# Kernel tuning notes

Measured on AMD Instinct MI355X. Metric: run time of the kernel, lower is better.

## Reference

```python
import jax, jax.numpy as jnp
import numpy as np

B, JX, JQ, D = 16, 4096, 512, 256
VERY_NEG = -1e30


def setup_inputs() -> dict:
    key = jax.random.key(0)
    ks = jax.random.split(key, 8)
    c = jax.random.normal(ks[0], (B, JX, D), dtype=jnp.float32)
    q = jax.random.normal(ks[1], (B, JQ, D), dtype=jnp.float32)
    # glorot-ish scaled weights for [4d, d] projections
    s = 1.0 / np.sqrt(4 * D)
    Wr = jax.random.normal(ks[2], (4 * D, D), dtype=jnp.float32) * s
    Wg = jax.random.normal(ks[3], (4 * D, D), dtype=jnp.float32) * s
    Br = jnp.zeros((D,), dtype=jnp.float32)
    Bg = jnp.zeros((D,), dtype=jnp.float32)
    # padding masks from random valid lengths (realistic ragged batch)
    c_len = jax.random.randint(ks[4], (B,), JX // 2, JX + 1)
    q_len = jax.random.randint(ks[5], (B,), JQ // 2, JQ + 1)
    c_mask = jnp.arange(JX)[None, :] < c_len[:, None]
    q_mask = jnp.arange(JQ)[None, :] < q_len[:, None]
    return {"c": c, "q": q, "Wr": Wr, "Br": Br, "Wg": Wg, "Bg": Bg,
            "c_mask": c_mask, "q_mask": q_mask}


def reference(c, q, Wr, Br, Wg, Bg, c_mask, q_mask):
    # logits[b,x,j] = <c[b,x], q[b,j]>
    logits = jnp.einsum('bxd,bjd->bxj', c, q)
    # exp_mask: add VERY_NEG where (c_mask & q_mask) is False
    cq_mask = c_mask[:, :, None] & q_mask[:, None, :]  # [B,JX,JQ]
    logits = logits + (1.0 - cq_mask.astype(logits.dtype)) * VERY_NEG
    a = jax.nn.softmax(logits, axis=-1)                # [B,JX,JQ]
    q_a = jnp.einsum('bxj,bjd->bxd', a, q)             # [B,JX,D]
    # semantic fusion unit
    cc = jnp.concatenate([c, q_a, c * q_a, c - q_a], axis=-1)  # [B,JX,4D]
    r_ = jnp.tanh(cc @ Wr + Br)
    g = jax.nn.sigmoid(cc @ Wg + Bg)
    return g * r_ + (1.0 - g) * c
```

## Files before the change

kernel.cpp:

```cpp
#include <hip/hip_runtime.h>
#include <hip/hip_bf16.h>
#include <stdint.h>

#define NB 16
#define JXX 4096
#define JQQ 512
#define DDD 256
#define LOG2E 1.44269504f

typedef __attribute__((ext_vector_type(8))) _Float16 f16x8;
typedef __attribute__((ext_vector_type(4))) _Float16 f16x4;
typedef __attribute__((ext_vector_type(4))) float f32x4;

__device__ __forceinline__ uint16_t f2h(float f) {
    union { _Float16 h; uint16_t s; } u; u.h = (_Float16)f; return u.s;
}
__device__ __forceinline__ float h2f(uint16_t s) {
    union { _Float16 h; uint16_t s; } u; u.s = s; return (float)u.h;
}

__device__ __forceinline__ void gload_lds16(const void* g, void* l) {
    __builtin_amdgcn_global_load_lds(
        (const __attribute__((address_space(1))) void*)g,
        (__attribute__((address_space(3))) void*)l, 16, 0, 0);
}

#define VMW(N) asm volatile("s_waitcnt vmcnt(" #N ")" ::: "memory")

__global__ void k_prep(const void* cmask, const void* qmask,
                       const float* __restrict__ qg,
                       const float* __restrict__ Wr, const float* __restrict__ Wg,
                       uint8_t* cm8, uint8_t* qm8,
                       uint16_t* __restrict__ qS, uint16_t* __restrict__ qTS,
                       uint16_t* __restrict__ WP3) {
    __shared__ __align__(16) char smem[16896];
    const int blk = blockIdx.x;
    const int t = threadIdx.x;

    if (blk < 256) {
        int i = blk * 256 + t;
        uint32_t w0c = *(const uint32_t*)cmask;
        uint32_t w0q = *(const uint32_t*)qmask;
        int mc = (w0c == 1u) ? 1 : (w0c == 0x3f800000u ? 2 : 0);
        int mq = (w0q == 1u) ? 1 : (w0q == 0x3f800000u ? 2 : 0);
        if (i < NB * JXX) {
            uint8_t v;
            if (mc == 1)      v = ((const int*)cmask)[i] != 0;
            else if (mc == 2) v = ((const float*)cmask)[i] != 0.0f;
            else              v = ((const uint8_t*)cmask)[i] != 0;
            cm8[i] = v;
        }
        if (i < NB * JQQ) {
            uint8_t v;
            if (mq == 1)      v = ((const int*)qmask)[i] != 0;
            else if (mq == 2) v = ((const float*)qmask)[i] != 0.0f;
            else              v = ((const uint8_t*)qmask)[i] != 0;
            qm8[i] = v;
        }
    } else if (blk < 768) {
        float (*tile)[65] = (float (*)[65])smem;
        const int idx = blk - 256;
        const int b = idx >> 5, jb = idx & 7, db = (idx & 31) >> 3;
        const int j0 = jb * 64, d0 = db * 64;
        #pragma unroll
        for (int i = 0; i < 16; i++) {
            int e = t + 256 * i;
            int r = e >> 6, c = e & 63;
            tile[r][c] = qg[((long)b * JQQ + j0 + r) * DDD + d0 + c];
        }
        __syncthreads();
        #pragma unroll
        for (int i = 0; i < 2; i++) {
            int e = t + 256 * i;
            int r = e >> 3, c8 = e & 7;
            f16x8 v;
            #pragma unroll
            for (int k = 0; k < 8; k++) v[k] = (_Float16)tile[r][c8 * 8 + k];
            int jt = (j0 >> 5) + (r >> 5);
            int row = r & 31;
            int d8 = (d0 >> 3) + c8;
            int byt = ((row * 512 + d8 * 16) ^ ((row & 7) << 4));
            *(f16x8*)(qS + ((long)(b * 16 + jt)) * 8192 + (byt >> 1)) = v;
        }
        #pragma unroll
        for (int i = 0; i < 2; i++) {
            int e = t + 256 * i;
            int dd = e >> 3, j8 = e & 7;
            f16x8 v;
            #pragma unroll
            for (int k = 0; k < 8; k++) v[k] = (_Float16)tile[j8 * 8 + k][dd];
            int jt = (j0 >> 5) + (j8 >> 2);
            int d = d0 + dd;
            int byt = ((d * 64 + (j8 & 3) * 16) ^ (((d >> 1) & 3) << 4));
            *(f16x8*)(qTS + ((long)(b * 16 + jt)) * 8192 + (byt >> 1)) = v;
        }
    } else {
        _Float16* tile = (_Float16*)smem;
        const int idx = blk - 768;
        const int ktl = idx & 7, rem = idx >> 3;
        const int comp = rem % 3, rg = rem / 3;
        const float* W = rg ? Wg : Wr;
        const int base0 = (comp == 0 ? 0 : comp == 1 ? 256 : 512) + ktl * 32;
        #pragma unroll
        for (int i = 0; i < 32; i++) {
            int e = t + 256 * i;
            int r = e >> 8, ccol = e & 255;
            float v = W[(long)(base0 + r) * 256 + ccol];
            if (comp == 0)      v += W[(long)(768 + ktl * 32 + r) * 256 + ccol];
            else if (comp == 1) v -= W[(long)(768 + ktl * 32 + r) * 256 + ccol];
            tile[r * 264 + ccol] = (_Float16)v;
        }
        __syncthreads();
        const int step = ktl * 3 + comp;
        #pragma unroll
        for (int ss = 0; ss < 4; ss++) {
            int slot = ss * 256 + t;
            int ntg = slot >> 6, lane = slot & 63;
            int gg = lane >> 4, l = lane & 15;
            f16x8 v;
            #pragma unroll
            for (int i = 0; i < 8; i++) v[i] = tile[(gg * 8 + i) * 264 + ntg * 16 + l];
            int hh = ntg >> 3, ntl = ntg & 7;
            long off = (long)step * 16384 + hh * 8192 + rg * 4096 + ntl * 512 + lane * 8;
            *(f16x8*)(WP3 + off) = v;
        }
    }
}

__global__ __launch_bounds__(256, 2) void k_attn(
    const float* __restrict__ cg,
    const uint16_t* __restrict__ qS,
    const uint16_t* __restrict__ qTS,
    const uint8_t* __restrict__ cm8,
    const uint8_t* __restrict__ qm8,
    uint16_t* __restrict__ qa16,
    uint16_t* __restrict__ c16)
{
    __shared__ __align__(16) uint16_t qbuf[2][8192];
    __shared__ __align__(16) uint16_t qTbuf[2][8192];
    __shared__ __align__(16) uint16_t P_lds[4 * 32 * 40];
    __shared__ __align__(16) uint32_t qm_lds[128];

    const int b = blockIdx.y;
    const int t = threadIdx.x;
    const int wave = t >> 6;
    const int lane = t & 63;
    const int l15 = lane & 15;
    const int g = lane >> 4;
    const int xw = blockIdx.x * 128 + wave * 32;

    if (t < 128) {
        uint32_t m = ((const uint32_t*)(qm8 + (long)b * JQQ))[t];
        qm_lds[t] = m;
    }

    f16x8 cfrag[2][8];
    bool cvalid[2];
    float m_run[2], s_run[2];
    #pragma unroll
    for (int xs = 0; xs < 2; xs++) {
        const long rowg = (long)b * JXX + xw + xs * 16 + l15;
        const float* crow = cg + rowg * DDD;
        uint16_t* c16row = c16 + rowg * DDD;
        #pragma unroll
        for (int kb = 0; kb < 8; kb++) {
            float4 v0 = *(const float4*)(crow + kb * 32 + g * 8);
            float4 v1 = *(const float4*)(crow + kb * 32 + g * 8 + 4);
            f16x8 f;
            f[0] = (_Float16)v0.x; f[1] = (_Float16)v0.y; f[2] = (_Float16)v0.z; f[3] = (_Float16)v0.w;
            f[4] = (_Float16)v1.x; f[5] = (_Float16)v1.y; f[6] = (_Float16)v1.z; f[7] = (_Float16)v1.w;
            cfrag[xs][kb] = f;
            *(f16x8*)(c16row + kb * 32 + g * 8) = f;
        }
        cvalid[xs] = cm8[rowg] != 0;
        m_run[xs] = cvalid[xs] ? -1e30f : 0.0f;
        s_run[xs] = 0.0f;
    }
    const f32x4 fzero = {0.f, 0.f, 0.f, 0.f};
    f32x4 qa[16][2];
    #pragma unroll
    for (int i = 0; i < 16; i++) { qa[i][0] = fzero; qa[i][1] = fzero; }

    const uint16_t* qSb  = qS  + (long)(b * 16) * 8192;
    const uint16_t* qTSb = qTS + (long)(b * 16) * 8192;

    const int kbit = (l15 >> 2) & 1;
    const int qbase = l15 * 256 + (((g * 16) ^ ((l15 & 3) << 4)) >> 1);
    const int qTbase = l15 * 32 + ((g ^ ((l15 >> 1) & 3)) * 8);

    #define STAGE_ATTN(bsel, tile)                                              \
        {                                                                       \
            const uint16_t* s1 = qSb + (long)(tile) * 8192;                     \
            const uint16_t* s2 = qTSb + (long)(tile) * 8192;                    \
            _Pragma("unroll")                                                   \
            for (int i = 0; i < 4; i++)                                         \
                gload_lds16(s1 + i * 2048 + t * 8,                              \
                            &qbuf[bsel][i * 2048 + wave * 512]);                \
            _Pragma("unroll")                                                   \
            for (int i = 0; i < 4; i++)                                         \
                gload_lds16(s2 + i * 2048 + t * 8,                              \
                            &qTbuf[bsel][i * 2048 + wave * 512]);               \
        }

    STAGE_ATTN(0, 0);
    asm volatile("s_waitcnt lgkmcnt(0)" ::: "memory");
    __builtin_amdgcn_s_barrier();

    int cur = 0;
    for (int jt = 0; jt < 16; jt++) {
        if (jt < 15) {
            STAGE_ATTN(cur ^ 1, jt + 1);
            VMW(8);
        } else {
            VMW(0);
        }
        __builtin_amdgcn_s_barrier();
        __builtin_amdgcn_sched_barrier(0);

        const uint16_t* qb_l  = &qbuf[cur][0];
        const uint16_t* qTb_l = &qTbuf[cur][0];

        uint32_t qmw[2];
        qmw[0] = qm_lds[jt * 8 + g];
        qmw[1] = qm_lds[jt * 8 + 4 + g];

        f32x4 acc[2][2];
        acc[0][0] = fzero; acc[0][1] = fzero; acc[1][0] = fzero; acc[1][1] = fzero;
        __builtin_amdgcn_s_setprio(1);
        #pragma unroll
        for (int js = 0; js < 2; js++) {
            #pragma unroll
            for (int kb = 0; kb < 8; kb++) {
                f16x8 qf = *(const f16x8*)(qb_l + js * 4096 + qbase + ((kb ^ kbit) << 5));
                acc[js][0] = __builtin_amdgcn_mfma_f32_16x16x32_f16(qf, cfrag[0][kb], acc[js][0], 0, 0, 0);
                acc[js][1] = __builtin_amdgcn_mfma_f32_16x16x32_f16(qf, cfrag[1][kb], acc[js][1], 0, 0, 0);
            }
        }
        __builtin_amdgcn_s_setprio(0);

        f16x4 pv[2][2];
        float fsc[2];
        #pragma unroll
        for (int xs = 0; xs < 2; xs++) {
            float lmax = -1e30f;
            #pragma unroll
            for (int js = 0; js < 2; js++) {
                #pragma unroll
                for (int r = 0; r < 4; r++) {
                    bool qv = (qmw[js] >> (8 * r)) & 0xffu;
                    lmax = fmaxf(lmax, qv ? acc[js][xs][r] : -1e30f);
                }
            }
            lmax = fmaxf(lmax, __shfl_xor(lmax, 16));
            lmax = fmaxf(lmax, __shfl_xor(lmax, 32));
            float m_new = cvalid[xs] ? ((lmax > m_run[xs] + 8.0f) ? lmax : m_run[xs]) : 0.0f;
            fsc[xs] = exp2f((m_run[xs] - m_new) * LOG2E);
            float psum = 0.0f;
            #pragma unroll
            for (int js = 0; js < 2; js++) {
                #pragma unroll
                for (int r = 0; r < 4; r++) {
                    bool qv = (qmw[js] >> (8 * r)) & 0xffu;
                    float p = qv ? exp2f((acc[js][xs][r] - m_new) * LOG2E) : 0.0f;
                    if (!cvalid[xs]) p = 1.0f;
                    psum += p;
                    pv[xs][js][r] = (_Float16)p;
                }
            }
            s_run[xs] = s_run[xs] * fsc[xs] + psum;
            m_run[xs] = m_new;
        }
        if (!__all(fsc[0] == 1.0f && fsc[1] == 1.0f)) {
            #pragma unroll
            for (int dt = 0; dt < 16; dt++) {
                #pragma unroll
                for (int xs = 0; xs < 2; xs++) {
                    qa[dt][xs][0] *= fsc[xs]; qa[dt][xs][1] *= fsc[xs];
                    qa[dt][xs][2] *= fsc[xs]; qa[dt][xs][3] *= fsc[xs];
                }
            }
        }

        uint16_t* Pw0 = P_lds + wave * 1280;
        #pragma unroll
        for (int xs = 0; xs < 2; xs++) {
            *(f16x4*)(Pw0 + (xs * 16 + l15) * 40 + g * 4) = pv[xs][0];
            *(f16x4*)(Pw0 + (xs * 16 + l15) * 40 + 16 + g * 4) = pv[xs][1];
        }
        f16x8 pa[2];
        pa[0] = *(const f16x8*)(Pw0 + l15 * 40 + g * 8);
        pa[1] = *(const f16x8*)(Pw0 + (16 + l15) * 40 + g * 8);

        __builtin_amdgcn_s_setprio(1);
        #pragma unroll
        for (int dt = 0; dt < 16; dt++) {
            f16x8 bq = *(const f16x8*)(qTb_l + qTbase + dt * 512);
            qa[dt][0] = __builtin_amdgcn_mfma_f32_16x16x32_f16(bq, pa[0], qa[dt][0], 0, 0, 0);
            qa[dt][1] = __builtin_amdgcn_mfma_f32_16x16x32_f16(bq, pa[1], qa[dt][1], 0, 0, 0);
        }
        __builtin_amdgcn_s_setprio(0);

        __builtin_amdgcn_sched_barrier(0);
        __builtin_amdgcn_s_barrier();
        cur ^= 1;
    }
    #undef STAGE_ATTN

    #pragma unroll
    for (int xs = 0; xs < 2; xs++) {
        float s_tot = s_run[xs] + __shfl_xor(s_run[xs], 16);
        s_tot = s_tot + __shfl_xor(s_tot, 32);
        float inv = 1.0f / s_tot;
        uint16_t* outp = qa16 + ((long)b * JXX + xw + xs * 16 + l15) * DDD;
        #pragma unroll
        for (int dt = 0; dt < 16; dt++) {
            f16x4 v;
            v[0] = (_Float16)(qa[dt][xs][0] * inv);
            v[1] = (_Float16)(qa[dt][xs][1] * inv);
            v[2] = (_Float16)(qa[dt][xs][2] * inv);
            v[3] = (_Float16)(qa[dt][xs][3] * inv);
            *(f16x4*)(outp + dt * 16 + g * 4) = v;
        }
    }
}

__global__ __launch_bounds__(256, 2) void k_sfu(
    const uint16_t* __restrict__ c16g,
    const uint16_t* __restrict__ qa16,
    const uint16_t* __restrict__ WP3,
    const float* __restrict__ Brb,
    const float* __restrict__ Bgb,
    float* __restrict__ outg)
{
    __shared__ __align__(16) uint16_t ab_lds[2][4096];
    __shared__ __align__(16) uint16_t wbuf[2][16384];

    const int t = threadIdx.x;
    const int wave = t >> 6, lane = t & 63;
    const int l15 = lane & 15, g = lane >> 4;
    const long m0 = (long)blockIdx.x * 64;

    const f32x4 fzero = {0.f, 0.f, 0.f, 0.f};
    f32x4 accR[4][4], accG[4][4];
    #pragma unroll
    for (int a = 0; a < 4; a++)
        #pragma unroll
        for (int bq = 0; bq < 4; bq++) { accR[a][bq] = fzero; accG[a][bq] = fzero; }

    const int wrd = (wave >> 1) * 8192 + (wave & 1) * 2048 + lane * 8;

    #define STAGE_CQA(dt_)                                                        \
        { _Pragma("unroll")                                                       \
          for (int j = 0; j < 2; j++) {                                           \
              int pp = j * 256 + t;                                               \
              int row = pp >> 3, pc = pp & 7;                                     \
              long src = (m0 + row) * 256 + (dt_) * 64 + ((pc ^ (row & 7)) << 3); \
              int dst = (j * 256 + wave * 64) * 8;                                \
              gload_lds16(c16g + src, &ab_lds[0][dst]);                           \
              gload_lds16(qa16 + src, &ab_lds[1][dst]);                           \
          } }

    #define STAGE_W(s_)                                                           \
        { _Pragma("unroll")                                                       \
          for (int i = 0; i < 8; i++)                                             \
              gload_lds16(WP3 + (long)(s_) * 16384 + i * 2048 + t * 8,            \
                          &wbuf[(s_) & 1][i * 2048 + wave * 512]); }

    STAGE_CQA(0);
    STAGE_W(0);
    VMW(0);
    __builtin_amdgcn_s_barrier();
    __builtin_amdgcn_sched_barrier(0);

    #pragma unroll
    for (int dt = 0; dt < 4; dt++) {
        #pragma unroll
        for (int kb = 0; kb < 2; kb++) {
            f16x8 cfr[4], qfr[4];
            #pragma unroll
            for (int mf = 0; mf < 4; mf++) {
                int row = mf * 16 + l15;
                int c8 = kb * 4 + g;
                int off = row * 64 + ((c8 ^ (row & 7)) << 3);
                cfr[mf] = *(const f16x8*)(&ab_lds[0][off]);
                qfr[mf] = *(const f16x8*)(&ab_lds[1][off]);
            }
            #pragma unroll
            for (int comp = 0; comp < 3; comp++) {
                const int s = dt * 6 + kb * 3 + comp;
                if (s < 23) STAGE_W(s + 1);
                if (dt < 3 && kb == 1 && comp == 1) STAGE_CQA(dt + 1);
                if (s == 23)                                   { VMW(0); }
                else if (dt < 3 && kb == 1 && comp == 1)       { VMW(12); }
                else                                           { VMW(8); }
                __builtin_amdgcn_s_barrier();
                __builtin_amdgcn_sched_barrier(0);
                f16x8 afc[4];
                #pragma unroll
                for (int mf = 0; mf < 4; mf++) {
                    if (comp == 0)      afc[mf] = cfr[mf];
                    else if (comp == 1) afc[mf] = qfr[mf];
                    else                afc[mf] = cfr[mf] * qfr[mf];
                }
                const uint16_t* Wb = &wbuf[s & 1][wrd];
                __builtin_amdgcn_s_setprio(1);
                #pragma unroll
                for (int nt = 0; nt < 4; nt++) {
                    f16x8 br = *(const f16x8*)(Wb + nt * 512);
                    f16x8 bg = *(const f16x8*)(Wb + 4096 + nt * 512);
                    #pragma unroll
                    for (int mf = 0; mf < 4; mf++) {
                        accR[mf][nt] = __builtin_amdgcn_mfma_f32_16x16x32_f16(afc[mf], br, accR[mf][nt], 0, 0, 0);
                        accG[mf][nt] = __builtin_amdgcn_mfma_f32_16x16x32_f16(afc[mf], bg, accG[mf][nt], 0, 0, 0);
                    }
                }
                __builtin_amdgcn_s_setprio(0);
                __builtin_amdgcn_sched_barrier(0);
                __builtin_amdgcn_s_barrier();
            }
        }
    }
    #undef STAGE_W
    #undef STAGE_CQA

    #pragma unroll
    for (int nt = 0; nt < 4; nt++) {
        int n = wave * 64 + nt * 16 + l15;
        float br = Brb[n], bg = Bgb[n];
        #pragma unroll
        for (int mf = 0; mf < 4; mf++) {
            long rowb = m0 + mf * 16 + g * 4;
            #pragma unroll
            for (int r = 0; r < 4; r++) {
                float pr = accR[mf][nt][r] + br;
                float pg = accG[mf][nt][r] + bg;
                float x = fminf(fmaxf(pr, -30.f), 30.f);
                float e2 = __expf(2.f * x);
                float rr = (e2 - 1.f) / (e2 + 1.f);
                float gv = 1.0f / (1.0f + __expf(-pg));
                float cv = h2f(c16g[(rowb + r) * DDD + n]);
                outg[(rowb + r) * DDD + n] = gv * rr + (1.f - gv) * cv;
            }
        }
    }
}

extern "C" void kernel_launch(void* const* d_in, const int* in_sizes, int n_in,
                              void* d_out, int out_size, void* d_ws, size_t ws_size,
                              hipStream_t stream) {
    const float* c  = (const float*)d_in[0];
    const float* q  = (const float*)d_in[1];
    const float* Wr = (const float*)d_in[2];
    const float* Br = (const float*)d_in[3];
    const float* Wg = (const float*)d_in[4];
    const float* Bg = (const float*)d_in[5];
    const void* cmask = d_in[6];
    const void* qmask = d_in[7];

    char* ws = (char*)d_ws;
    uint16_t* qS    = (uint16_t*)(ws + 0);
    uint16_t* qTS   = (uint16_t*)(ws + 4194304);
    uint16_t* qa16  = (uint16_t*)(ws + 8388608);
    uint16_t* c16   = (uint16_t*)(ws + 41943040);
    uint16_t* WP3   = (uint16_t*)(ws + 75497472);
    uint8_t*  cm8   = (uint8_t*)(ws + 77594624);
    uint8_t*  qm8   = (uint8_t*)(ws + 77660160);
    (void)in_sizes; (void)n_in; (void)out_size; (void)ws_size;

    k_prep<<<dim3(816), dim3(256), 0, stream>>>(cmask, qmask, q, Wr, Wg,
                                                cm8, qm8, qS, qTS, WP3);
    k_attn<<<dim3(JXX / 128, NB), dim3(256), 0, stream>>>(c, qS, qTS, cm8, qm8, qa16, c16);
    k_sfu<<<dim3((NB * JXX) / 64), dim3(256), 0, stream>>>(
        c16, qa16, WP3, Br, Bg, (float*)d_out);
}
```

Baseline: 150.5 us.

## Single-buffer q tiles in LDS and split prefetch between the two GEMM phases

Replaces the double-buffered q and qT LDS tiles with single buffers. The next q tile is now prefetched once the QK^T MFMAs finish, and the next qT tile once the PV MFMAs finish, with extra barriers between phases. This roughly halves the staging LDS footprint, which may allow more resident blocks. In exchange it adds four barriers per iteration and gives the loads less time to overlap with compute. The vmcnt thresholds look permissive, so there is some risk of reading a tile before its load has landed.

```diff
diff --git a/kernel.cpp b/kernel.cpp
--- a/kernel.cpp
+++ b/kernel.cpp
@@ -136,8 +136,8 @@
     uint16_t* __restrict__ qa16,
     uint16_t* __restrict__ c16)
 {
-    __shared__ __align__(16) uint16_t qbuf[2][8192];
-    __shared__ __align__(16) uint16_t qTbuf[2][8192];
+    __shared__ __align__(16) uint16_t qbuf[8192];
+    __shared__ __align__(16) uint16_t qTbuf[8192];
     __shared__ __align__(16) uint16_t P_lds[4 * 32 * 40];
     __shared__ __align__(16) uint32_t qm_lds[128];
 
@@ -188,38 +188,24 @@
     const int qbase = l15 * 256 + (((g * 16) ^ ((l15 & 3) << 4)) >> 1);
     const int qTbase = l15 * 32 + ((g ^ ((l15 >> 1) & 3)) * 8);
 
-    #define STAGE_ATTN(bsel, tile)                                              \
-        {                                                                       \
-            const uint16_t* s1 = qSb + (long)(tile) * 8192;                     \
-            const uint16_t* s2 = qTSb + (long)(tile) * 8192;                    \
-            _Pragma("unroll")                                                   \
-            for (int i = 0; i < 4; i++)                                         \
-                gload_lds16(s1 + i * 2048 + t * 8,                              \
-                            &qbuf[bsel][i * 2048 + wave * 512]);                \
-            _Pragma("unroll")                                                   \
-            for (int i = 0; i < 4; i++)                                         \
-                gload_lds16(s2 + i * 2048 + t * 8,                              \
-                            &qTbuf[bsel][i * 2048 + wave * 512]);               \
-        }
-
-    STAGE_ATTN(0, 0);
-    asm volatile("s_waitcnt lgkmcnt(0)" ::: "memory");
+    #define STAGE_QS(tile)                                                      \
+        { const uint16_t* s1 = qSb + (long)(tile) * 8192;                       \
+          _Pragma("unroll")                                                     \
+          for (int i = 0; i < 4; i++)                                           \
+              gload_lds16(s1 + i * 2048 + t * 8, &qbuf[i * 2048 + wave * 512]); }
+    #define STAGE_QT(tile)                                                      \
+        { const uint16_t* s2 = qTSb + (long)(tile) * 8192;                      \
+          _Pragma("unroll")                                                     \
+          for (int i = 0; i < 4; i++)                                           \
+              gload_lds16(s2 + i * 2048 + t * 8, &qTbuf[i * 2048 + wave * 512]); }
+
+    STAGE_QS(0);
+    STAGE_QT(0);
+    VMW(8);
     __builtin_amdgcn_s_barrier();
-
-    int cur = 0;
+    __builtin_amdgcn_sched_barrier(0);
+
     for (int jt = 0; jt < 16; jt++) {
-        if (jt < 15) {
-            STAGE_ATTN(cur ^ 1, jt + 1);
-            VMW(8);
-        } else {
-            VMW(0);
-        }
-        __builtin_amdgcn_s_barrier();
-        __builtin_amdgcn_sched_barrier(0);
-
-        const uint16_t* qb_l  = &qbuf[cur][0];
-        const uint16_t* qTb_l = &qTbuf[cur][0];
-
         uint32_t qmw[2];
         qmw[0] = qm_lds[jt * 8 + g];
         qmw[1] = qm_lds[jt * 8 + 4 + g];
@@ -231,12 +217,16 @@
         for (int js = 0; js < 2; js++) {
             #pragma unroll
             for (int kb = 0; kb < 8; kb++) {
-                f16x8 qf = *(const f16x8*)(qb_l + js * 4096 + qbase + ((kb ^ kbit) << 5));
+                f16x8 qf = *(const f16x8*)(&qbuf[js * 4096 + qbase + ((kb ^ kbit) << 5)]);
                 acc[js][0] = __builtin_amdgcn_mfma_f32_16x16x32_f16(qf, cfrag[0][kb], acc[js][0], 0, 0, 0);
                 acc[js][1] = __builtin_amdgcn_mfma_f32_16x16x32_f16(qf, cfrag[1][kb], acc[js][1], 0, 0, 0);
             }
         }
         __builtin_amdgcn_s_setprio(0);
+        __builtin_amdgcn_sched_barrier(0);
+        __builtin_amdgcn_s_barrier();
+        __builtin_amdgcn_sched_barrier(0);
+        if (jt < 15) STAGE_QS(jt + 1);
 
         f16x4 pv[2][2];
         float fsc[2];
@@ -291,20 +281,30 @@
         pa[0] = *(const f16x8*)(Pw0 + l15 * 40 + g * 8);
         pa[1] = *(const f16x8*)(Pw0 + (16 + l15) * 40 + g * 8);
 
+        if (jt < 15) { VMW(8); } else { VMW(0); }
+        __builtin_amdgcn_s_barrier();
+        __builtin_amdgcn_sched_barrier(0);
+
         __builtin_amdgcn_s_setprio(1);
         #pragma unroll
         for (int dt = 0; dt < 16; dt++) {
-            f16x8 bq = *(const f16x8*)(qTb_l + qTbase + dt * 512);
+            f16x8 bq = *(const f16x8*)(&qTbuf[qTbase + dt * 512]);
             qa[dt][0] = __builtin_amdgcn_mfma_f32_16x16x32_f16(bq, pa[0], qa[dt][0], 0, 0, 0);
             qa[dt][1] = __builtin_amdgcn_mfma_f32_16x16x32_f16(bq, pa[1], qa[dt][1], 0, 0, 0);
         }
         __builtin_amdgcn_s_setprio(0);
-
         __builtin_amdgcn_sched_barrier(0);
         __builtin_amdgcn_s_barrier();
-        cur ^= 1;
-    }
-    #undef STAGE_ATTN
+        __builtin_amdgcn_sched_barrier(0);
+        if (jt < 15) {
+            STAGE_QT(jt + 1);
+            VMW(8);
+        }
+        __builtin_amdgcn_s_barrier();
+        __builtin_amdgcn_sched_barrier(0);
+    }
+    #undef STAGE_QS
+    #undef STAGE_QT
 
     #pragma unroll
     for (int xs = 0; xs < 2; xs++) {
```

New measurement: 149.8 us (median of 2 runs). Within noise of the previous version (-0.4%).
